# Kernel tuning notes

Hardware: AMD Instinct MI355X
Metric: run time of the kernel (lower is better)

## Reference

```python
import jax, jax.numpy as jnp
import numpy as np

BS, N, NP, K = 2, 4096, 1024, 8   # batch, fine pts, coarse pts, in-degree per fine node
CI, CO, MID = 32, 16, 32          # in channels (16 skip + 16 interpolated), out channels, radial MLP width
E = BS * N * K


def setup_inputs() -> dict:
    key = jax.random.key(0)
    ks = iter(jax.random.split(key, 64))
    nrm = lambda s, sc=1.0: jax.random.normal(next(ks), s, jnp.float32) * sc
    inp = {}
    inp['h0'] = nrm((BS * N, 16, 1))
    inp['h1'] = nrm((BS * N, 16, 3))
    inp['uph0'] = nrm((BS * NP, 16, 1))
    inp['uph1'] = nrm((BS * NP, 16, 3))
    inp['xyz'] = jax.random.uniform(next(ks), (BS, N, 3), jnp.float32)
    inp['xyz_prev'] = jax.random.uniform(next(ks), (BS, NP, 3), jnp.float32)
    dst = jnp.repeat(jnp.arange(BS * N, dtype=jnp.int32), K)
    src = (dst // N) * N + jax.random.randint(next(ks), (E,), 0, N, jnp.int32)
    inp['edge_src'], inp['edge_dst'] = src, dst
    xf = inp['xyz'].reshape(BS * N, 3)
    inp['r'] = jnp.linalg.norm(xf[src] - xf[dst], axis=-1, keepdims=True)
    # CG basis tensors basis[din,dout]: [E, 2*dout+1, 2*din+1, 2*min(din,dout)+1]
    inp['basis00'] = nrm((E, 1, 1, 1))
    inp['basis01'] = nrm((E, 3, 1, 1))
    inp['basis10'] = nrm((E, 1, 3, 1))
    inp['basis11'] = nrm((E, 3, 3, 3))
    for p, f in (('00', 1), ('01', 1), ('10', 1), ('11', 3)):
        inp['rw1_' + p] = nrm((1, MID), 0.5)
        inp['rb1_' + p] = jnp.zeros((MID,), jnp.float32)
        inp['rw2_' + p] = nrm((MID, MID), 0.2)
        inp['rb2_' + p] = jnp.zeros((MID,), jnp.float32)
        inp['rw3_' + p] = nrm((MID, CO * CI * f), 0.1)
    inp['wself0'] = nrm((CO, CI), 0.1)
    inp['wself1'] = nrm((CO, CI), 0.1)
    inp['gamma0'] = jnp.ones((CO,), jnp.float32)
    inp['beta0'] = jnp.zeros((CO,), jnp.float32)
    inp['gamma1'] = jnp.ones((CO,), jnp.float32)
    inp['beta1'] = jnp.zeros((CO,), jnp.float32)
    return inp


def _radial(r, w1, b1, w2, b2, w3, f):
    x = jax.nn.relu(r @ w1 + b1)
    x = jax.nn.relu(x @ w2 + b2)
    return (x @ w3).reshape(E, CO, CI, f)


def _pair_msg(basis, hsrc, R):
    # basis [E,mo,mi,f], hsrc [E,ci,mi], R [E,co,ci,f] -> msg [E,co,mo]
    # (fused form of per-edge kernel = sum_f R*basis followed by kernel @ src)
    tmp = jnp.einsum('emnf,ein->eimf', basis, hsrc)
    return jnp.einsum('eoif,eimf->eom', R, tmp)


def _gnorm(h, gamma, beta):
    # GNormSE3: norm over m-dim, LayerNorm+ReLU on norms, rescale phase
    n = jnp.sqrt(jnp.sum(h * h, -1) + 1e-12)           # [Nn,co]
    phase = h / n[..., None]
    mu = jnp.mean(n, -1, keepdims=True)
    var = jnp.var(n, -1, keepdims=True)
    t = jax.nn.relu((n - mu) / jnp.sqrt(var + 1e-5) * gamma + beta)
    return t[..., None] * phase


def _fwd(h0, h1, uph0, uph1, xyz, xyz_prev, r, basis00, basis01, basis10, basis11,
         rw1_00, rb1_00, rw2_00, rb2_00, rw3_00,
         rw1_01, rb1_01, rw2_01, rb2_01, rw3_01,
         rw1_10, rb1_10, rw2_10, rb2_10, rw3_10,
         rw1_11, rb1_11, rw2_11, rb2_11, rw3_11,
         wself0, wself1, gamma0, beta0, gamma1, beta1, edge_src, edge_dst):
    # --- three_nn + inverse-squared-distance interpolation of coarse features ---
    d2 = jnp.sum((xyz[:, :, None, :] - xyz_prev[:, None, :, :]) ** 2, -1)  # [B,N,NP]
    negd, idx = jax.lax.top_k(-d2, 3)
    dist = jnp.sqrt(jnp.maximum(-negd, 0.0))
    d2c = jnp.maximum(dist * dist, 1e-10)
    inv = 1.0 / (d2c + 1e-8)
    w = inv / jnp.sum(inv, -1, keepdims=True)          # [B,N,3]

    def interp(uph):
        C, F = uph.shape[1], uph.shape[2]
        fp = uph.reshape(BS, NP, C * F)
        g = jax.vmap(lambda f_, i_: f_[i_])(fp, idx)   # [B,N,3,C*F]
        return jnp.sum(g * w[..., None], 2).reshape(BS * N, C, F)

    h0c = jnp.concatenate([interp(uph0), h0], 1)       # [BN,CI,1]
    h1c = jnp.concatenate([interp(uph1), h1], 1)       # [BN,CI,3]

    # --- GConvSE3: per-edge CG-basis kernels, mean aggregation, self-interaction ---
    hs0, hs1 = h0c[edge_src], h1c[edge_src]
    R00 = _radial(r, rw1_00, rb1_00, rw2_00, rb2_00, rw3_00, 1)
    R01 = _radial(r, rw1_01, rb1_01, rw2_01, rb2_01, rw3_01, 1)
    R10 = _radial(r, rw1_10, rb1_10, rw2_10, rb2_10, rw3_10, 1)
    R11 = _radial(r, rw1_11, rb1_11, rw2_11, rb2_11, rw3_11, 3)
    msg0 = _pair_msg(basis00, hs0, R00) + _pair_msg(basis10, hs1, R10)  # [E,CO,1]
    msg1 = _pair_msg(basis01, hs0, R01) + _pair_msg(basis11, hs1, R11)  # [E,CO,3]
    agg0 = jax.ops.segment_sum(msg0, edge_dst, num_segments=BS * N) / K  # mean (in-degree K)
    agg1 = jax.ops.segment_sum(msg1, edge_dst, num_segments=BS * N) / K
    out0 = agg0 + jnp.einsum('oi,nim->nom', wself0, h0c)
    out1 = agg1 + jnp.einsum('oi,nim->nom', wself1, h1c)

    return _gnorm(out0, gamma0, beta0), _gnorm(out1, gamma1, beta1)


def reference(h0, h1, uph0, uph1, xyz, xyz_prev, r, basis00, basis01, basis10, basis11,
              rw1_00, rb1_00, rw2_00, rb2_00, rw3_00,
              rw1_01, rb1_01, rw2_01, rb2_01, rw3_01,
              rw1_10, rb1_10, rw2_10, rb2_10, rw3_10,
              rw1_11, rb1_11, rw2_11, rb2_11, rw3_11,
              wself0, wself1, gamma0, beta0, gamma1, beta1, edge_src, edge_dst):
    return _fwd(h0, h1, uph0, uph1, xyz, xyz_prev, r, basis00, basis01, basis10, basis11,
                rw1_00, rb1_00, rw2_00, rb2_00, rw3_00,
                rw1_01, rb1_01, rw2_01, rb2_01, rw3_01,
                rw1_10, rb1_10, rw2_10, rb2_10, rw3_10,
                rw1_11, rb1_11, rw2_11, rb2_11, rw3_11,
                wself0, wself1, gamma0, beta0, gamma1, beta1, edge_src, edge_dst)
```

## Files before the change

kernel.cpp:

```cpp
#include <hip/hip_runtime.h>
#include <hip/hip_bf16.h>
#include <hip/hip_fp16.h>
#include <math.h>

#define NPP   1024
#define BN    8192
#define NE    65536

typedef __attribute__((ext_vector_type(8))) short bf16x8;
typedef __attribute__((ext_vector_type(4))) float f32x4;

__device__ __forceinline__ short f2bf(float f) {
  __hip_bfloat16 h = __float2bfloat16(f);
  return *reinterpret_cast<short*>(&h);
}
__device__ __forceinline__ float b2f(short h) {
  unsigned u = ((unsigned)(unsigned short)h) << 16;
  return __uint_as_float(u);
}
__device__ __forceinline__ unsigned short f2h(float f) {
  __half h = __float2half(f);
  return *reinterpret_cast<unsigned short*>(&h);
}
__device__ __forceinline__ float h2f(unsigned short u) {
  __half h = *reinterpret_cast<__half*>(&u);
  return __half2float(h);
}

__device__ __forceinline__ unsigned long long pkkey(float d, int j) {
  return ((unsigned long long)__float_as_uint(d) << 32) | (unsigned int)j;
}

__global__ __launch_bounds__(256) void interp_kernel(
    const float* __restrict__ h0, const float* __restrict__ h1,
    const float* __restrict__ uph0, const float* __restrict__ uph1,
    const float* __restrict__ xyz, const float* __restrict__ xyzp,
    float* __restrict__ h0c, float* __restrict__ h1c)
{
  const int tid  = threadIdx.x;
  const int lane = tid & 63;
  const int wid  = tid >> 6;
  const int fi   = blockIdx.x * 4 + wid;
  const int b    = fi >> 12;

  const float px = xyz[fi*3+0], py = xyz[fi*3+1], pz = xyz[fi*3+2];

  unsigned long long k0 = ~0ull, k1 = ~0ull, k2 = ~0ull;
  const float* cbase = xyzp + (size_t)b*NPP*3;
  #pragma unroll 4
  for (int j = lane; j < NPP; j += 64) {
    const float* cp = cbase + j*3;
    float ax = px - cp[0], ay = py - cp[1], az = pz - cp[2];
    float dd = fmaf(az, az, fmaf(ay, ay, ax*ax));
    unsigned long long kk = pkkey(dd, j);
    if (kk < k0)      { k2 = k1; k1 = k0; k0 = kk; }
    else if (kk < k1) { k2 = k1; k1 = kk; }
    else if (kk < k2) { k2 = kk; }
  }
  #pragma unroll
  for (int off = 1; off < 64; off <<= 1) {
    unsigned long long b0 = __shfl_xor(k0, off);
    unsigned long long b1 = __shfl_xor(k1, off);
    unsigned long long b2 = __shfl_xor(k2, off);
    unsigned long long c0, c1, c2;
    if (k0 <= b0) {
      c0 = k0;
      if (k1 <= b0) { c1 = k1; c2 = (k2 <= b0) ? k2 : b0; }
      else          { c1 = b0; c2 = (k1 <= b1) ? k1 : b1; }
    } else {
      c0 = b0;
      if (b1 <= k0) { c1 = b1; c2 = (b2 <= k0) ? b2 : k0; }
      else          { c1 = k0; c2 = (b1 <= k1) ? b1 : k1; }
    }
    k0 = c0; k1 = c1; k2 = c2;
  }
  const int i0 = (int)(k0 & 0xffffffffu);
  const int i1 = (int)(k1 & 0xffffffffu);
  const int i2 = (int)(k2 & 0xffffffffu);
  const float dd0 = __uint_as_float((unsigned)(k0 >> 32));
  const float dd1 = __uint_as_float((unsigned)(k1 >> 32));
  const float dd2 = __uint_as_float((unsigned)(k2 >> 32));

  float w0, w1v, w2v;
  {
    float s0 = sqrtf(fmaxf(dd0, 0.f));
    float s1 = sqrtf(fmaxf(dd1, 0.f));
    float s2 = sqrtf(fmaxf(dd2, 0.f));
    w0  = 1.f / (fmaxf(s0*s0, 1e-10f) + 1e-8f);
    w1v = 1.f / (fmaxf(s1*s1, 1e-10f) + 1e-8f);
    w2v = 1.f / (fmaxf(s2*s2, 1e-10f) + 1e-8f);
    float wsum = w0 + w1v + w2v;
    w0 /= wsum; w1v /= wsum; w2v /= wsum;
  }

  const float* u0 = uph0 + (size_t)b*NPP*16;
  const float* u1 = uph1 + (size_t)b*NPP*48;
  if (lane < 16) {
    int c = lane;
    h0c[(size_t)fi*32 + c] = w0*u0[i0*16+c] + w1v*u0[i1*16+c] + w2v*u0[i2*16+c];
    h0c[(size_t)fi*32 + 16 + c] = h0[(size_t)fi*16 + c];
  } else {
    int q = lane - 16;
    h1c[(size_t)fi*96 + q] = w0*u1[i0*48+q] + w1v*u1[i1*48+q] + w2v*u1[i2*48+q];
    h1c[(size_t)fi*96 + 48 + q] = h1[(size_t)fi*48 + q];
  }
}

__global__ __launch_bounds__(256) void repack_bf16(
    const float* __restrict__ w00, const float* __restrict__ w01,
    const float* __restrict__ w10, const float* __restrict__ w11,
    const float* __restrict__ w2_00, const float* __restrict__ w2_01,
    const float* __restrict__ w2_10, const float* __restrict__ w2_11,
    unsigned short* __restrict__ B00, unsigned short* __restrict__ B01,
    unsigned short* __restrict__ B10, unsigned short* __restrict__ B11,
    unsigned short* __restrict__ W2H, unsigned short* __restrict__ W2L)
{
  int idx = blockIdx.x * 256 + threadIdx.x;
  if (idx < 49152) {
    int a = idx & 16383;
    int i = a & 31, o = (a >> 5) & 15, k = a >> 9;
    int src = k*512 + o*32 + i;
    if (idx < 16384)      B00[a] = (unsigned short)f2bf(w00[src]);
    else if (idx < 32768) B01[a] = (unsigned short)f2bf(w01[src]);
    else                  B10[a] = (unsigned short)f2bf(w10[src]);
  } else if (idx < 98304) {
    int a = idx - 49152;
    int i = a & 31, o = (a >> 5) & 15, s = a >> 9;
    int f = s >> 5, k = s & 31;
    B11[a] = (unsigned short)f2bf(w11[k*1536 + (o*32+i)*3 + f]);
  } else if (idx < 102400) {
    int a = idx - 98304;
    int p = a >> 10, rem = a & 1023;
    int b = rem >> 5, aa = rem & 31;
    const float* w2p = p==0?w2_00 : p==1?w2_01 : p==2?w2_10 : w2_11;
    W2H[a] = (unsigned short)f2bf(w2p[aa*32 + b]);
  } else if (idx < 106496) {
    int a = idx - 102400;
    int p = a >> 10, rem = a & 1023;
    int b = rem >> 5, aa = rem & 31;
    const float* w2p = p==0?w2_00 : p==1?w2_01 : p==2?w2_10 : w2_11;
    float v = w2p[aa*32 + b];
    short h = f2bf(v);
    W2L[a] = (unsigned short)f2bf(v - b2f(h));
  }
}

struct EP {
  const float *r; const int *esrc;
  const float *b00, *b01, *b10, *b11;
  const float *w1_00, *b1_00, *b2_00;
  const float *w1_01, *b1_01, *b2_01;
  const float *w1_10, *b1_10, *b2_10;
  const float *w1_11, *b1_11, *b2_11;
  const unsigned short *B00, *B01, *B10, *B11, *W2H, *W2L;
  const float *h0c, *h1c;
  float *agg0, *agg1;
};

#define CVT4(PTR) ({ ushort4 u_ = *(const ushort4*)(PTR); \
    f32x4 r_; r_[0]=h2f(u_.x); r_[1]=h2f(u_.y); r_[2]=h2f(u_.z); r_[3]=h2f(u_.w); r_; })

__global__ __launch_bounds__(256) void edge_mfma(EP P)
{
  __shared__ __align__(16) unsigned short x2Lh[32*264];

  const int tid  = threadIdx.x;
  const int wid  = tid >> 6;
  const int lane = tid & 63;
  const int el   = lane & 15;
  const int kg   = lane >> 4;
  const int kg4  = kg << 2;
  const int eb   = blockIdx.x * 64 + wid * 16;
  const int e    = eb + el;
  const int isl  = kg * 8;

  const int   sidx = P.esrc[e];
  const float rv   = P.r[e];

  const f32x4 zero4 = {0.f, 0.f, 0.f, 0.f};

  #pragma unroll
  for (int p = 0; p < 4; ++p) {
    const float* w1p = p==0?P.w1_00 : p==1?P.w1_01 : p==2?P.w1_10 : P.w1_11;
    const float* b1p = p==0?P.b1_00 : p==1?P.b1_01 : p==2?P.b1_10 : P.b1_11;
    const float* b2p = p==0?P.b2_00 : p==1?P.b2_01 : p==2?P.b2_10 : P.b2_11;
    const unsigned short* w2hp = P.W2H + p*1024;
    const unsigned short* w2lp = P.W2L + p*1024;
    f32x4 wa  = *(const f32x4*)(w1p + isl);
    f32x4 wb  = *(const f32x4*)(w1p + isl + 4);
    f32x4 ba  = *(const f32x4*)(b1p + isl);
    f32x4 bbv = *(const f32x4*)(b1p + isl + 4);
    bf16x8 bh0 = *(const bf16x8*)(w2hp + el*32 + isl);
    bf16x8 bh1 = *(const bf16x8*)(w2hp + (16+el)*32 + isl);
    bf16x8 bl0 = *(const bf16x8*)(w2lp + el*32 + isl);
    bf16x8 bl1 = *(const bf16x8*)(w2lp + (16+el)*32 + isl);
    float b2v0 = b2p[el];
    float b2v1 = b2p[16 + el];
    bf16x8 axh, axl;
    #pragma unroll
    for (int j = 0; j < 4; ++j) {
      float v0 = fmaxf(fmaf(rv, wa[j], ba[j]),  0.f);
      float v1 = fmaxf(fmaf(rv, wb[j], bbv[j]), 0.f);
      short h0s = f2bf(v0), h1s_ = f2bf(v1);
      axh[j]   = h0s;  axl[j]   = f2bf(v0 - b2f(h0s));
      axh[j+4] = h1s_; axl[j+4] = f2bf(v1 - b2f(h1s_));
    }
    f32x4 z0 = __builtin_amdgcn_mfma_f32_16x16x32_bf16(axl, bh0, zero4, 0,0,0);
    z0 = __builtin_amdgcn_mfma_f32_16x16x32_bf16(axh, bl0, z0, 0,0,0);
    z0 = __builtin_amdgcn_mfma_f32_16x16x32_bf16(axh, bh0, z0, 0,0,0);
    f32x4 z1 = __builtin_amdgcn_mfma_f32_16x16x32_bf16(axl, bh1, zero4, 0,0,0);
    z1 = __builtin_amdgcn_mfma_f32_16x16x32_bf16(axh, bl1, z1, 0,0,0);
    z1 = __builtin_amdgcn_mfma_f32_16x16x32_bf16(axh, bh1, z1, 0,0,0);
    ushort4 o0, o1v;
    o0.x  = f2h(fmaxf(z0[0] + b2v0, 0.f));
    o0.y  = f2h(fmaxf(z0[1] + b2v0, 0.f));
    o0.z  = f2h(fmaxf(z0[2] + b2v0, 0.f));
    o0.w  = f2h(fmaxf(z0[3] + b2v0, 0.f));
    o1v.x = f2h(fmaxf(z1[0] + b2v1, 0.f));
    o1v.y = f2h(fmaxf(z1[1] + b2v1, 0.f));
    o1v.z = f2h(fmaxf(z1[2] + b2v1, 0.f));
    o1v.w = f2h(fmaxf(z1[3] + b2v1, 0.f));
    *(ushort4*)&x2Lh[el*264      + wid*64 + p*16 + kg4] = o0;
    *(ushort4*)&x2Lh[(16+el)*264 + wid*64 + p*16 + kg4] = o1v;
  }

  f32x4 h0a = *(const f32x4*)(P.h0c + (size_t)sidx*32 + isl);
  f32x4 h0b = *(const f32x4*)(P.h0c + (size_t)sidx*32 + isl + 4);
  float h1sl[24];
  {
    const float* hp = P.h1c + (size_t)sidx*96 + isl*3;
    #pragma unroll
    for (int q = 0; q < 6; ++q) {
      f32x4 v = *(const f32x4*)(hp + q*4);
      h1sl[q*4+0]=v[0]; h1sl[q*4+1]=v[1]; h1sl[q*4+2]=v[2]; h1sl[q*4+3]=v[3];
    }
  }

  bf16x8 a_h0;
  #pragma unroll
  for (int j = 0; j < 4; ++j) { a_h0[j] = f2bf(h0a[j]); a_h0[j+4] = f2bf(h0b[j]); }

  const int xrow = wid*64 + kg4;

  f32x4 macc0 = zero4;
  {
    const unsigned short* bb = P.B00 + el*32 + isl;
    #pragma unroll 4
    for (int t = 0; t < 32; ++t) {
      bf16x8 bv = *(const bf16x8*)(bb + t*512);
      f32x4 z = __builtin_amdgcn_mfma_f32_16x16x32_bf16(a_h0, bv, zero4, 0, 0, 0);
      f32x4 xs = CVT4(&x2Lh[t*264 + xrow + 0]);
      macc0[0] = fmaf(xs[0], z[0], macc0[0]);
      macc0[1] = fmaf(xs[1], z[1], macc0[1]);
      macc0[2] = fmaf(xs[2], z[2], macc0[2]);
      macc0[3] = fmaf(xs[3], z[3], macc0[3]);
    }
  }
  {
    f32x4 bv = *(const f32x4*)(P.b00 + eb + kg4);
    macc0[0]*=bv[0]; macc0[1]*=bv[1]; macc0[2]*=bv[2]; macc0[3]*=bv[3];
  }

  {
    const float* bp = P.b10 + (size_t)e*3;
    float c0 = bp[0], c1 = bp[1], c2 = bp[2];
    bf16x8 a_t;
    #pragma unroll
    for (int j = 0; j < 8; ++j)
      a_t[j] = f2bf(c0*h1sl[j*3+0] + c1*h1sl[j*3+1] + c2*h1sl[j*3+2]);
    const unsigned short* bb = P.B10 + el*32 + isl;
    #pragma unroll 4
    for (int t = 0; t < 32; ++t) {
      bf16x8 bv = *(const bf16x8*)(bb + t*512);
      f32x4 z = __builtin_amdgcn_mfma_f32_16x16x32_bf16(a_t, bv, zero4, 0, 0, 0);
      f32x4 xs = CVT4(&x2Lh[t*264 + xrow + 32]);
      macc0[0] = fmaf(xs[0], z[0], macc0[0]);
      macc0[1] = fmaf(xs[1], z[1], macc0[1]);
      macc0[2] = fmaf(xs[2], z[2], macc0[2]);
      macc0[3] = fmaf(xs[3], z[3], macc0[3]);
    }
  }
  {
    float s = macc0[0]+macc0[1]+macc0[2]+macc0[3];
    s += __shfl_xor(s, 16);
    if ((kg & 1) == 0)
      P.agg0[(size_t)((eb >> 3) + (kg >> 1))*16 + el] = s * 0.125f;
  }

  f32x4 c01 = zero4;
  {
    const unsigned short* bb = P.B01 + el*32 + isl;
    #pragma unroll 4
    for (int t = 0; t < 32; ++t) {
      bf16x8 bv = *(const bf16x8*)(bb + t*512);
      f32x4 z = __builtin_amdgcn_mfma_f32_16x16x32_bf16(a_h0, bv, zero4, 0, 0, 0);
      f32x4 xs = CVT4(&x2Lh[t*264 + xrow + 16]);
      c01[0] = fmaf(xs[0], z[0], c01[0]);
      c01[1] = fmaf(xs[1], z[1], c01[1]);
      c01[2] = fmaf(xs[2], z[2], c01[2]);
      c01[3] = fmaf(xs[3], z[3], c01[3]);
    }
  }
  f32x4 m1a, m1b, m1c;
  {
    const float* bp = P.b01 + (size_t)(eb + kg4)*3;
    f32x4 q0 = *(const f32x4*)(bp);
    f32x4 q1 = *(const f32x4*)(bp + 4);
    f32x4 q2 = *(const f32x4*)(bp + 8);
    m1a[0]=c01[0]*q0[0]; m1a[1]=c01[1]*q0[3]; m1a[2]=c01[2]*q1[2]; m1a[3]=c01[3]*q2[1];
    m1b[0]=c01[0]*q0[1]; m1b[1]=c01[1]*q1[0]; m1b[2]=c01[2]*q1[3]; m1b[3]=c01[3]*q2[2];
    m1c[0]=c01[0]*q0[2]; m1c[1]=c01[1]*q1[1]; m1c[2]=c01[2]*q2[0]; m1c[3]=c01[3]*q2[3];
  }

  {
    const float* b11e = P.b11 + (size_t)e*27;
    #pragma unroll 1
    for (int f = 0; f < 3; ++f) {
      float bm[9];
      #pragma unroll
      for (int mn = 0; mn < 9; ++mn) bm[mn] = b11e[mn*3 + f];
      bf16x8 am0, am1, am2;
      #pragma unroll
      for (int j = 0; j < 8; ++j) {
        float hn0 = h1sl[j*3+0], hn1 = h1sl[j*3+1], hn2 = h1sl[j*3+2];
        am0[j] = f2bf(bm[0]*hn0 + bm[1]*hn1 + bm[2]*hn2);
        am1[j] = f2bf(bm[3]*hn0 + bm[4]*hn1 + bm[5]*hn2);
        am2[j] = f2bf(bm[6]*hn0 + bm[7]*hn1 + bm[8]*hn2);
      }
      const unsigned short* bb = P.B11 + (size_t)f*16384 + el*32 + isl;
      #pragma unroll 4
      for (int t = 0; t < 32; ++t) {
        bf16x8 bv = *(const bf16x8*)(bb + t*512);
        f32x4 z0 = __builtin_amdgcn_mfma_f32_16x16x32_bf16(am0, bv, zero4, 0, 0, 0);
        f32x4 z1 = __builtin_amdgcn_mfma_f32_16x16x32_bf16(am1, bv, zero4, 0, 0, 0);
        f32x4 z2 = __builtin_amdgcn_mfma_f32_16x16x32_bf16(am2, bv, zero4, 0, 0, 0);
        f32x4 xs = CVT4(&x2Lh[t*264 + xrow + 48]);
        m1a[0] = fmaf(xs[0], z0[0], m1a[0]);
        m1a[1] = fmaf(xs[1], z0[1], m1a[1]);
        m1a[2] = fmaf(xs[2], z0[2], m1a[2]);
        m1a[3] = fmaf(xs[3], z0[3], m1a[3]);
        m1b[0] = fmaf(xs[0], z1[0], m1b[0]);
        m1b[1] = fmaf(xs[1], z1[1], m1b[1]);
        m1b[2] = fmaf(xs[2], z1[2], m1b[2]);
        m1b[3] = fmaf(xs[3], z1[3], m1b[3]);
        m1c[0] = fmaf(xs[0], z2[0], m1c[0]);
        m1c[1] = fmaf(xs[1], z2[1], m1c[1]);
        m1c[2] = fmaf(xs[2], z2[2], m1c[2]);
        m1c[3] = fmaf(xs[3], z2[3], m1c[3]);
      }
    }
  }

  {
    float sa = m1a[0]+m1a[1]+m1a[2]+m1a[3]; sa += __shfl_xor(sa, 16);
    float sb = m1b[0]+m1b[1]+m1b[2]+m1b[3]; sb += __shfl_xor(sb, 16);
    float sc = m1c[0]+m1c[1]+m1c[2]+m1c[3]; sc += __shfl_xor(sc, 16);
    if ((kg & 1) == 0) {
      float* p = P.agg1 + (size_t)((eb >> 3) + (kg >> 1))*48 + el*3;
      p[0] = sa * 0.125f; p[1] = sb * 0.125f; p[2] = sc * 0.125f;
    }
  }
}

__global__ __launch_bounds__(256) void gnorm_kernel(
    const float* __restrict__ agg0, const float* __restrict__ agg1,
    const float* __restrict__ h0c, const float* __restrict__ h1c,
    const float* __restrict__ ws0, const float* __restrict__ ws1,
    const float* __restrict__ g0, const float* __restrict__ be0,
    const float* __restrict__ g1, const float* __restrict__ be1,
    float* __restrict__ out)
{
  const int gt  = blockIdx.x * 256 + threadIdx.x;
  const int fi  = gt >> 2;
  const int t4  = gt & 3;
  const int ob  = t4 * 4;

  const float* h0p = h0c + (size_t)fi*32;
  const float* h1p = h1c + (size_t)fi*96;

  float o0[4];
  #pragma unroll
  for (int oo = 0; oo < 4; ++oo) {
    int o = ob + oo;
    float a = agg0[(size_t)fi*16 + o];
    #pragma unroll
    for (int i = 0; i < 32; ++i)
      a = fmaf(ws0[o*32+i], h0p[i], a);
    o0[oo] = a;
  }
  {
    float n0[4], lmu = 0.f;
    #pragma unroll
    for (int oo = 0; oo < 4; ++oo) { n0[oo] = sqrtf(fmaf(o0[oo], o0[oo], 1e-12f)); lmu += n0[oo]; }
    lmu += __shfl_xor(lmu, 1); lmu += __shfl_xor(lmu, 2);
    float mu = lmu * 0.0625f;
    float lv = 0.f;
    #pragma unroll
    for (int oo = 0; oo < 4; ++oo) { float d = n0[oo]-mu; lv = fmaf(d, d, lv); }
    lv += __shfl_xor(lv, 1); lv += __shfl_xor(lv, 2);
    float inv = 1.f / sqrtf(lv * 0.0625f + 1e-5f);
    #pragma unroll
    for (int oo = 0; oo < 4; ++oo) {
      int o = ob + oo;
      float t = fmaxf(fmaf((n0[oo]-mu)*inv, g0[o], be0[o]), 0.f);
      out[(size_t)fi*16 + o] = t * (o0[oo] / n0[oo]);
    }
  }

  float o1[12];
  #pragma unroll
  for (int oo = 0; oo < 4; ++oo) {
    int o = ob + oo;
    float a0 = agg1[(size_t)fi*48 + o*3+0];
    float a1 = agg1[(size_t)fi*48 + o*3+1];
    float a2 = agg1[(size_t)fi*48 + o*3+2];
    #pragma unroll
    for (int i = 0; i < 32; ++i) {
      float wv = ws1[o*32+i];
      a0 = fmaf(wv, h1p[i*3+0], a0);
      a1 = fmaf(wv, h1p[i*3+1], a1);
      a2 = fmaf(wv, h1p[i*3+2], a2);
    }
    o1[oo*3+0] = a0; o1[oo*3+1] = a1; o1[oo*3+2] = a2;
  }
  {
    float n1[4], lmu = 0.f;
    #pragma unroll
    for (int oo = 0; oo < 4; ++oo) {
      float s = fmaf(o1[oo*3+0], o1[oo*3+0], 1e-12f);
      s = fmaf(o1[oo*3+1], o1[oo*3+1], s);
      s = fmaf(o1[oo*3+2], o1[oo*3+2], s);
      n1[oo] = sqrtf(s); lmu += n1[oo];
    }
    lmu += __shfl_xor(lmu, 1); lmu += __shfl_xor(lmu, 2);
    float mu = lmu * 0.0625f;
    float lv = 0.f;
    #pragma unroll
    for (int oo = 0; oo < 4; ++oo) { float d = n1[oo]-mu; lv = fmaf(d, d, lv); }
    lv += __shfl_xor(lv, 1); lv += __shfl_xor(lv, 2);
    float inv = 1.f / sqrtf(lv * 0.0625f + 1e-5f);
    float* out1 = out + (size_t)BN*16;
    #pragma unroll
    for (int oo = 0; oo < 4; ++oo) {
      int o = ob + oo;
      float t = fmaxf(fmaf((n1[oo]-mu)*inv, g1[o], be1[o]), 0.f);
      #pragma unroll
      for (int m = 0; m < 3; ++m)
        out1[(size_t)fi*48 + o*3+m] = t * (o1[oo*3+m] / n1[oo]);
    }
  }
}

extern "C" void kernel_launch(void* const* d_in, const int* in_sizes, int n_in,
                              void* d_out, int out_size, void* d_ws, size_t ws_size,
                              hipStream_t stream)
{
  (void)in_sizes; (void)n_in; (void)out_size; (void)ws_size;
  const float* h0   = (const float*)d_in[0];
  const float* h1   = (const float*)d_in[1];
  const float* uph0 = (const float*)d_in[2];
  const float* uph1 = (const float*)d_in[3];
  const float* xyz  = (const float*)d_in[4];
  const float* xyzp = (const float*)d_in[5];
  const int*   esrc = (const int*)d_in[6];
  const float* rr   = (const float*)d_in[8];

  float* wsp  = (float*)d_ws;
  float* h0c  = wsp;
  float* h1c  = h0c + (size_t)BN*32;
  float* agg0 = h1c + (size_t)BN*96;
  float* agg1 = agg0 + (size_t)BN*16;
  unsigned short* B00 = (unsigned short*)(agg1 + (size_t)BN*48);
  unsigned short* B01 = B00 + 16384;
  unsigned short* B10 = B01 + 16384;
  unsigned short* B11 = B10 + 16384;
  unsigned short* W2H = B11 + 49152;
  unsigned short* W2L = W2H + 4096;

  interp_kernel<<<BN/4, 256, 0, stream>>>(h0, h1, uph0, uph1, xyz, xyzp, h0c, h1c);
  repack_bf16<<<416, 256, 0, stream>>>(
      (const float*)d_in[17], (const float*)d_in[22],
      (const float*)d_in[27], (const float*)d_in[32],
      (const float*)d_in[15], (const float*)d_in[20],
      (const float*)d_in[25], (const float*)d_in[30],
      B00, B01, B10, B11, W2H, W2L);

  EP P;
  P.r = rr; P.esrc = esrc;
  P.b00 = (const float*)d_in[9];  P.b01 = (const float*)d_in[10];
  P.b10 = (const float*)d_in[11]; P.b11 = (const float*)d_in[12];
  P.w1_00 = (const float*)d_in[13]; P.b1_00 = (const float*)d_in[14]; P.b2_00 = (const float*)d_in[16];
  P.w1_01 = (const float*)d_in[18]; P.b1_01 = (const float*)d_in[19]; P.b2_01 = (const float*)d_in[21];
  P.w1_10 = (const float*)d_in[23]; P.b1_10 = (const float*)d_in[24]; P.b2_10 = (const float*)d_in[26];
  P.w1_11 = (const float*)d_in[28]; P.b1_11 = (const float*)d_in[29]; P.b2_11 = (const float*)d_in[31];
  P.B00 = B00; P.B01 = B01; P.B10 = B10; P.B11 = B11; P.W2H = W2H; P.W2L = W2L;
  P.h0c = h0c; P.h1c = h1c; P.agg0 = agg0; P.agg1 = agg1;

  edge_mfma<<<NE/64, 256, 0, stream>>>(P);

  gnorm_kernel<<<BN*4/256, 256, 0, stream>>>(agg0, agg1, h0c, h1c,
      (const float*)d_in[33], (const float*)d_in[34],
      (const float*)d_in[35], (const float*)d_in[36],
      (const float*)d_in[37], (const float*)d_in[38],
      (float*)d_out);
}
```

Measured before the change: 104.9 us.

## Split the MID reduction across two waves per edge group with LDS reduction

Each block now runs 512 threads. Two waves share a 16-edge group, and each computes half of the 32 MID hidden channels of the radial MLP and half of the t-loop contractions. The partial accumulators from the second wave are reduced through shared memory, with barriers, before the first wave writes the aggregated outputs. The aim is to double the parallelism and halve each wave's serial MFMA/FMA chain to improve latency hiding. In exchange it adds two block syncs and an LDS reduction pass, and raises per-block register pressure.

```diff
diff --git a/kernel.cpp b/kernel.cpp
--- a/kernel.cpp
+++ b/kernel.cpp
@@ -160,19 +160,23 @@
 #define CVT4(PTR) ({ ushort4 u_ = *(const ushort4*)(PTR); \
     f32x4 r_; r_[0]=h2f(u_.x); r_[1]=h2f(u_.y); r_[2]=h2f(u_.z); r_[3]=h2f(u_.w); r_; })
 
-__global__ __launch_bounds__(256) void edge_mfma(EP P)
+__global__ __launch_bounds__(512) void edge_mfma(EP P)
 {
-  __shared__ __align__(16) unsigned short x2Lh[32*264];
+  __shared__ __align__(16) unsigned short x2Lh[16*544];
 
   const int tid  = threadIdx.x;
-  const int wid  = tid >> 6;
+  const int w    = tid >> 6;
   const int lane = tid & 63;
   const int el   = lane & 15;
   const int kg   = lane >> 4;
   const int kg4  = kg << 2;
-  const int eb   = blockIdx.x * 64 + wid * 16;
+  const int isl  = kg * 8;
+  const int eg   = w >> 1;
+  const int th   = w & 1;
+  const int eb   = blockIdx.x * 64 + eg * 16;
   const int e    = eb + el;
-  const int isl  = kg * 8;
+  const int ch   = th*16 + el;
+  const int tb   = th * 16;
 
   const int   sidx = P.esrc[e];
   const float rv   = P.r[e];
@@ -184,18 +188,15 @@
     const float* w1p = p==0?P.w1_00 : p==1?P.w1_01 : p==2?P.w1_10 : P.w1_11;
     const float* b1p = p==0?P.b1_00 : p==1?P.b1_01 : p==2?P.b1_10 : P.b1_11;
     const float* b2p = p==0?P.b2_00 : p==1?P.b2_01 : p==2?P.b2_10 : P.b2_11;
-    const unsigned short* w2hp = P.W2H + p*1024;
-    const unsigned short* w2lp = P.W2L + p*1024;
+    const unsigned short* bhp = P.W2H + p*1024 + ch*32 + isl;
+    const unsigned short* blp = P.W2L + p*1024 + ch*32 + isl;
     f32x4 wa  = *(const f32x4*)(w1p + isl);
     f32x4 wb  = *(const f32x4*)(w1p + isl + 4);
     f32x4 ba  = *(const f32x4*)(b1p + isl);
     f32x4 bbv = *(const f32x4*)(b1p + isl + 4);
-    bf16x8 bh0 = *(const bf16x8*)(w2hp + el*32 + isl);
-    bf16x8 bh1 = *(const bf16x8*)(w2hp + (16+el)*32 + isl);
-    bf16x8 bl0 = *(const bf16x8*)(w2lp + el*32 + isl);
-    bf16x8 bl1 = *(const bf16x8*)(w2lp + (16+el)*32 + isl);
-    float b2v0 = b2p[el];
-    float b2v1 = b2p[16 + el];
+    bf16x8 bh = *(const bf16x8*)bhp;
+    bf16x8 bl = *(const bf16x8*)blp;
+    float b2v = b2p[ch];
     bf16x8 axh, axl;
     #pragma unroll
     for (int j = 0; j < 4; ++j) {
@@ -205,23 +206,15 @@
       axh[j]   = h0s;  axl[j]   = f2bf(v0 - b2f(h0s));
       axh[j+4] = h1s_; axl[j+4] = f2bf(v1 - b2f(h1s_));
     }
-    f32x4 z0 = __builtin_amdgcn_mfma_f32_16x16x32_bf16(axl, bh0, zero4, 0,0,0);
-    z0 = __builtin_amdgcn_mfma_f32_16x16x32_bf16(axh, bl0, z0, 0,0,0);
-    z0 = __builtin_amdgcn_mfma_f32_16x16x32_bf16(axh, bh0, z0, 0,0,0);
-    f32x4 z1 = __builtin_amdgcn_mfma_f32_16x16x32_bf16(axl, bh1, zero4, 0,0,0);
-    z1 = __builtin_amdgcn_mfma_f32_16x16x32_bf16(axh, bl1, z1, 0,0,0);
-    z1 = __builtin_amdgcn_mfma_f32_16x16x32_bf16(axh, bh1, z1, 0,0,0);
-    ushort4 o0, o1v;
-    o0.x  = f2h(fmaxf(z0[0] + b2v0, 0.f));
-    o0.y  = f2h(fmaxf(z0[1] + b2v0, 0.f));
-    o0.z  = f2h(fmaxf(z0[2] + b2v0, 0.f));
-    o0.w  = f2h(fmaxf(z0[3] + b2v0, 0.f));
-    o1v.x = f2h(fmaxf(z1[0] + b2v1, 0.f));
-    o1v.y = f2h(fmaxf(z1[1] + b2v1, 0.f));
-    o1v.z = f2h(fmaxf(z1[2] + b2v1, 0.f));
-    o1v.w = f2h(fmaxf(z1[3] + b2v1, 0.f));
-    *(ushort4*)&x2Lh[el*264      + wid*64 + p*16 + kg4] = o0;
-    *(ushort4*)&x2Lh[(16+el)*264 + wid*64 + p*16 + kg4] = o1v;
+    f32x4 z = __builtin_amdgcn_mfma_f32_16x16x32_bf16(axl, bh, zero4, 0,0,0);
+    z = __builtin_amdgcn_mfma_f32_16x16x32_bf16(axh, bl, z, 0,0,0);
+    z = __builtin_amdgcn_mfma_f32_16x16x32_bf16(axh, bh, z, 0,0,0);
+    ushort4 ov;
+    ov.x = f2h(fmaxf(z[0] + b2v, 0.f));
+    ov.y = f2h(fmaxf(z[1] + b2v, 0.f));
+    ov.z = f2h(fmaxf(z[2] + b2v, 0.f));
+    ov.w = f2h(fmaxf(z[3] + b2v, 0.f));
+    *(ushort4*)&x2Lh[el*544 + w*64 + p*16 + kg4] = ov;
   }
 
   f32x4 h0a = *(const f32x4*)(P.h0c + (size_t)sidx*32 + isl);
@@ -240,16 +233,16 @@
   #pragma unroll
   for (int j = 0; j < 4; ++j) { a_h0[j] = f2bf(h0a[j]); a_h0[j+4] = f2bf(h0b[j]); }
 
-  const int xrow = wid*64 + kg4;
+  const int xrow = w*64 + kg4;
 
   f32x4 macc0 = zero4;
   {
-    const unsigned short* bb = P.B00 + el*32 + isl;
+    const unsigned short* bb = P.B00 + (size_t)tb*512 + el*32 + isl;
     #pragma unroll 4
-    for (int t = 0; t < 32; ++t) {
+    for (int t = 0; t < 16; ++t) {
       bf16x8 bv = *(const bf16x8*)(bb + t*512);
       f32x4 z = __builtin_amdgcn_mfma_f32_16x16x32_bf16(a_h0, bv, zero4, 0, 0, 0);
-      f32x4 xs = CVT4(&x2Lh[t*264 + xrow + 0]);
+      f32x4 xs = CVT4(&x2Lh[t*544 + xrow + 0]);
       macc0[0] = fmaf(xs[0], z[0], macc0[0]);
       macc0[1] = fmaf(xs[1], z[1], macc0[1]);
       macc0[2] = fmaf(xs[2], z[2], macc0[2]);
@@ -268,33 +261,27 @@
     #pragma unroll
     for (int j = 0; j < 8; ++j)
       a_t[j] = f2bf(c0*h1sl[j*3+0] + c1*h1sl[j*3+1] + c2*h1sl[j*3+2]);
-    const unsigned short* bb = P.B10 + el*32 + isl;
+    const unsigned short* bb = P.B10 + (size_t)tb*512 + el*32 + isl;
     #pragma unroll 4
-    for (int t = 0; t < 32; ++t) {
+    for (int t = 0; t < 16; ++t) {
       bf16x8 bv = *(const bf16x8*)(bb + t*512);
       f32x4 z = __builtin_amdgcn_mfma_f32_16x16x32_bf16(a_t, bv, zero4, 0, 0, 0);
-      f32x4 xs = CVT4(&x2Lh[t*264 + xrow + 32]);
+      f32x4 xs = CVT4(&x2Lh[t*544 + xrow + 32]);
       macc0[0] = fmaf(xs[0], z[0], macc0[0]);
       macc0[1] = fmaf(xs[1], z[1], macc0[1]);
       macc0[2] = fmaf(xs[2], z[2], macc0[2]);
       macc0[3] = fmaf(xs[3], z[3], macc0[3]);
     }
   }
-  {
-    float s = macc0[0]+macc0[1]+macc0[2]+macc0[3];
-    s += __shfl_xor(s, 16);
-    if ((kg & 1) == 0)
-      P.agg0[(size_t)((eb >> 3) + (kg >> 1))*16 + el] = s * 0.125f;
-  }
 
   f32x4 c01 = zero4;
   {
-    const unsigned short* bb = P.B01 + el*32 + isl;
+    const unsigned short* bb = P.B01 + (size_t)tb*512 + el*32 + isl;
     #pragma unroll 4
-    for (int t = 0; t < 32; ++t) {
+    for (int t = 0; t < 16; ++t) {
       bf16x8 bv = *(const bf16x8*)(bb + t*512);
       f32x4 z = __builtin_amdgcn_mfma_f32_16x16x32_bf16(a_h0, bv, zero4, 0, 0, 0);
-      f32x4 xs = CVT4(&x2Lh[t*264 + xrow + 16]);
+      f32x4 xs = CVT4(&x2Lh[t*544 + xrow + 16]);
       c01[0] = fmaf(xs[0], z[0], c01[0]);
       c01[1] = fmaf(xs[1], z[1], c01[1]);
       c01[2] = fmaf(xs[2], z[2], c01[2]);
@@ -327,14 +314,14 @@
         am1[j] = f2bf(bm[3]*hn0 + bm[4]*hn1 + bm[5]*hn2);
         am2[j] = f2bf(bm[6]*hn0 + bm[7]*hn1 + bm[8]*hn2);
       }
-      const unsigned short* bb = P.B11 + (size_t)f*16384 + el*32 + isl;
+      const unsigned short* bb = P.B11 + (size_t)f*16384 + (size_t)tb*512 + el*32 + isl;
       #pragma unroll 4
-      for (int t = 0; t < 32; ++t) {
+      for (int t = 0; t < 16; ++t) {
         bf16x8 bv = *(const bf16x8*)(bb + t*512);
         f32x4 z0 = __builtin_amdgcn_mfma_f32_16x16x32_bf16(am0, bv, zero4, 0, 0, 0);
         f32x4 z1 = __builtin_amdgcn_mfma_f32_16x16x32_bf16(am1, bv, zero4, 0, 0, 0);
         f32x4 z2 = __builtin_amdgcn_mfma_f32_16x16x32_bf16(am2, bv, zero4, 0, 0, 0);
-        f32x4 xs = CVT4(&x2Lh[t*264 + xrow + 48]);
+        f32x4 xs = CVT4(&x2Lh[t*544 + xrow + 48]);
         m1a[0] = fmaf(xs[0], z0[0], m1a[0]);
         m1a[1] = fmaf(xs[1], z0[1], m1a[1]);
         m1a[2] = fmaf(xs[2], z0[2], m1a[2]);
@@ -351,7 +338,29 @@
     }
   }
 
-  {
+  __syncthreads();
+  float* red = (float*)x2Lh;
+  const int rbase = (eg*64 + lane)*17;
+  if (th == 1) {
+    float* rp = red + rbase;
+    rp[0]=macc0[0]; rp[1]=macc0[1]; rp[2]=macc0[2]; rp[3]=macc0[3];
+    rp[4]=m1a[0]; rp[5]=m1a[1]; rp[6]=m1a[2]; rp[7]=m1a[3];
+    rp[8]=m1b[0]; rp[9]=m1b[1]; rp[10]=m1b[2]; rp[11]=m1b[3];
+    rp[12]=m1c[0]; rp[13]=m1c[1]; rp[14]=m1c[2]; rp[15]=m1c[3];
+  }
+  __syncthreads();
+  if (th == 0) {
+    const float* rp = red + rbase;
+    macc0[0]+=rp[0]; macc0[1]+=rp[1]; macc0[2]+=rp[2]; macc0[3]+=rp[3];
+    m1a[0]+=rp[4]; m1a[1]+=rp[5]; m1a[2]+=rp[6]; m1a[3]+=rp[7];
+    m1b[0]+=rp[8]; m1b[1]+=rp[9]; m1b[2]+=rp[10]; m1b[3]+=rp[11];
+    m1c[0]+=rp[12]; m1c[1]+=rp[13]; m1c[2]+=rp[14]; m1c[3]+=rp[15];
+
+    float s = macc0[0]+macc0[1]+macc0[2]+macc0[3];
+    s += __shfl_xor(s, 16);
+    if ((kg & 1) == 0)
+      P.agg0[(size_t)((eb >> 3) + (kg >> 1))*16 + el] = s * 0.125f;
+
     float sa = m1a[0]+m1a[1]+m1a[2]+m1a[3]; sa += __shfl_xor(sa, 16);
     float sb = m1b[0]+m1b[1]+m1b[2]+m1b[3]; sb += __shfl_xor(sb, 16);
     float sc = m1c[0]+m1c[1]+m1c[2]+m1c[3]; sc += __shfl_xor(sc, 16);
@@ -496,7 +505,7 @@
   P.B00 = B00; P.B01 = B01; P.B10 = B10; P.B11 = B11; P.W2H = W2H; P.W2L = W2L;
   P.h0c = h0c; P.h1c = h1c; P.agg0 = agg0; P.agg1 = agg1;
 
-  edge_mfma<<<NE/64, 256, 0, stream>>>(P);
+  edge_mfma<<<NE/64, 512, 0, stream>>>(P);
 
   gnorm_kernel<<<BN*4/256, 256, 0, stream>>>(agg0, agg1, h0c, h1c,
       (const float*)d_in[33], (const float*)d_in[34],
```

New measurement: 109.7 us. 4.5% more time.
